# Kernel optimization log

Hardware: AMD Instinct MI355X
Metric: run time of the kernel (lower is better)

## Reference

```python
import jax, jax.numpy as jnp
import numpy as np

DIM = 256; INNER = 512; HEADS = 8; DHEAD = 64; WS = 7; K = 3; EPS = 1e-5

def _rel_idx(ws):
    idx = np.array([[x, y] for x in range(ws) for y in range(ws)])
    d = idx[None, :, :] - idx[:, None, :]
    d[:, :, 0] += ws - 1
    d[:, :, 1] += ws - 1
    d[:, :, 0] *= 2 * ws - 1
    return jnp.asarray(d.sum(-1))  # [ws^2, ws^2] int

REL_IDX = _rel_idx(WS)

def _proj(x, dw, g, b, m, v, pw):
    # depthwise conv (k=3, pad=1, groups=C) -> BN (eval mode) -> 1x1 pointwise
    p = K // 2
    y = jax.lax.conv_general_dilated(x, dw, (1, 1), ((p, p), (p, p)),
                                     feature_group_count=x.shape[1])
    y = (y - m[None, :, None, None]) * jax.lax.rsqrt(v[None, :, None, None] + EPS) \
        * g[None, :, None, None] + b[None, :, None, None]
    return jax.lax.conv_general_dilated(y, pw, (1, 1), 'VALID')

def _windows(t):
    # [b, h*d, H, W] -> [b, h, nw, ws*ws, d]  (non-shuffle partition)
    b, c, H, W = t.shape
    nh, nw = H // WS, W // WS
    t = t.reshape(b, HEADS, DHEAD, nh, WS, nw, WS)
    t = t.transpose(0, 1, 3, 5, 4, 6, 2)  # b h nh nw ws ws d
    return t.reshape(b, HEADS, nh * nw, WS * WS, DHEAD)

def _unwindows(t, H, W):
    b = t.shape[0]
    nh, nw = H // WS, W // WS
    t = t.reshape(b, HEADS, nh, nw, WS, WS, DHEAD)
    t = t.transpose(0, 1, 6, 2, 4, 3, 5)  # b h d nh ws nw ws
    return t.reshape(b, HEADS * DHEAD, H, W)

def setup_inputs() -> dict:
    key = jax.random.key(0)
    ks = jax.random.split(key, 32)
    d = {'x': jax.random.normal(ks[0], (16, DIM, 56, 56), jnp.float32)}
    i = 1
    for p in ('q', 'k', 'v'):
        d[p + '_dw'] = jax.random.normal(ks[i], (DIM, 1, K, K), jnp.float32) * 0.1; i += 1
        d[p + '_g'] = jax.random.uniform(ks[i], (DIM,), jnp.float32); i += 1
        d[p + '_b'] = jax.random.normal(ks[i], (DIM,), jnp.float32) * 0.1; i += 1
        d[p + '_m'] = jax.random.normal(ks[i], (DIM,), jnp.float32) * 0.1; i += 1
        d[p + '_v'] = jax.random.uniform(ks[i], (DIM,), jnp.float32); i += 1
        d[p + '_pw'] = jax.random.normal(ks[i], (INNER, DIM, 1, 1), jnp.float32) * 0.05; i += 1
    d['pos_emb'] = jax.random.normal(ks[i], ((2 * WS - 1) ** 2, HEADS), jnp.float32); i += 1
    d['out_w'] = jax.random.normal(ks[i], (DIM, INNER, 1, 1), jnp.float32) * 0.05; i += 1
    d['out_b'] = jax.random.normal(ks[i], (DIM,), jnp.float32) * 0.1
    return d

def reference(x, q_dw, q_g, q_b, q_m, q_v, q_pw,
              k_dw, k_g, k_b, k_m, k_v, k_pw,
              v_dw, v_g, v_b, v_m, v_v, v_pw,
              pos_emb, out_w, out_b):
    H, W = x.shape[2], x.shape[3]
    q = _windows(_proj(x, q_dw, q_g, q_b, q_m, q_v, q_pw))
    k = _windows(_proj(x, k_dw, k_g, k_b, k_m, k_v, k_pw))
    v = _windows(_proj(x, v_dw, v_g, v_b, v_m, v_v, v_pw))
    dots = jnp.einsum('bhwid,bhwjd->bhwij', q, k) * (DHEAD ** -0.5)
    bias = pos_emb[REL_IDX]              # [i, j, heads]
    dots = dots + bias.transpose(2, 0, 1)[None, :, None]  # broadcast over b, w
    attn = jax.nn.softmax(dots, axis=-1)
    out = jnp.einsum('bhwij,bhwjd->bhwid', attn, v)
    out = _unwindows(out, H, W)
    out = jax.lax.conv_general_dilated(out, out_w, (1, 1), 'VALID') \
          + out_b[None, :, None, None]
    return out
```

## Files before the change

### kernel.cpp

```cpp
#include <hip/hip_runtime.h>
#include <hip/hip_bf16.h>

typedef __hip_bfloat16 bf16;
typedef __bf16 bfv8 __attribute__((ext_vector_type(8)));
typedef float f32x4 __attribute__((ext_vector_type(4)));

constexpr int B_     = 16;
constexpr int C_     = 256;
constexpr int INNER_ = 512;
constexpr int HEADS_ = 8;
constexpr int DH_    = 64;
constexpr int HW_    = 56;
constexpr int NPIX_  = HW_ * HW_;
constexpr int WS_    = 7;
constexpr int WSQ_   = 49;
constexpr int NWIN_  = 64;

static __device__ __forceinline__ void async16(const void* g, void* l) {
    __builtin_amdgcn_global_load_lds(
        (const __attribute__((address_space(1))) unsigned int*)g,
        (__attribute__((address_space(3))) unsigned int*)l, 16, 0, 0);
}

__global__ __launch_bounds__(256) void setup_kernel(
    const float* __restrict__ pw0, const float* __restrict__ pw1,
    const float* __restrict__ pw2, const float* __restrict__ pw3,
    bf16* __restrict__ wq,
    const float* __restrict__ dw0, const float* __restrict__ g0,
    const float* __restrict__ b0, const float* __restrict__ m0,
    const float* __restrict__ v0,
    const float* __restrict__ dw1, const float* __restrict__ g1,
    const float* __restrict__ b1, const float* __restrict__ m1,
    const float* __restrict__ v1,
    const float* __restrict__ dw2, const float* __restrict__ g2,
    const float* __restrict__ b2, const float* __restrict__ m2,
    const float* __restrict__ v2,
    float* __restrict__ wf,
    const float* __restrict__ pos, float* __restrict__ biasf) {
    int bx = blockIdx.x;
    if (bx < 2048) {
        int g = bx >> 9;
        const float* s = g == 0 ? pw0 : (g == 1 ? pw1 : (g == 2 ? pw2 : pw3));
        int i = (bx & 511) * 256 + threadIdx.x;
        wq[(size_t)g * (INNER_ * C_) + i] = __float2bfloat16(s[i]);
    } else if (bx < 2051) {
        int p = bx - 2048, c = threadIdx.x;
        const float* dw = p == 0 ? dw0 : (p == 1 ? dw1 : dw2);
        const float* g  = p == 0 ? g0  : (p == 1 ? g1  : g2);
        const float* bb = p == 0 ? b0  : (p == 1 ? b1  : b2);
        const float* mm = p == 0 ? m0  : (p == 1 ? m1  : m2);
        const float* vv = p == 0 ? v0  : (p == 1 ? v1  : v2);
        float s = g[c] * rsqrtf(vv[c] + 1e-5f);
        float* o = wf + (size_t)(p * 256 + c) * 12;
#pragma unroll
        for (int k = 0; k < 9; ++k) o[k] = dw[c * 9 + k] * s;
        o[9] = bb[c] - mm[c] * s;
        o[10] = 0.f; o[11] = 0.f;
    } else {
        int h = bx - 2051;
        int wv = threadIdx.x >> 6, lane = threadIdx.x & 63;
        int quad = lane >> 4, col16 = lane & 15;
        float* dst = biasf + (((size_t)h * 4 + wv) * 64 + lane) * 16;
#pragma unroll
        for (int nt = 0; nt < 4; ++nt)
#pragma unroll
            for (int r = 0; r < 4; ++r) {
                int row = wv * 16 + quad * 4 + r;
                int col = nt * 16 + col16;
                float v;
                if (col >= WSQ_) v = -1e30f;
                else if (row >= WSQ_) v = 0.f;
                else {
                    int xi = row / WS_, yi = row % WS_;
                    int xj = col / WS_, yj = col % WS_;
                    int rel = (xj - xi + 6) * 13 + (yj - yi + 6);
                    v = pos[rel * HEADS_ + h];
                }
                dst[nt * 4 + r] = v;
            }
    }
}

__global__ __launch_bounds__(256) void dwbn3_kernel(
    const float* __restrict__ x, const float* __restrict__ wf,
    bf16* __restrict__ tq, bf16* __restrict__ tk, bf16* __restrict__ tv) {
    __shared__ float xs[3 * 64 * 61];
    int y  = blockIdx.x;
    int c0 = blockIdx.y * 64;
    int b  = blockIdx.z;
    int tid = threadIdx.x;
    for (int i = tid; i < 2688; i += 256) {
        int row = i / 896;
        int rem = i - row * 896;
        int ch = rem / 14, s = rem - ch * 14;
        int yy = y + row - 1;
        float4 v4 = make_float4(0.f, 0.f, 0.f, 0.f);
        if (yy >= 0 && yy < HW_)
            v4 = *(const float4*)(x + (size_t)(b * C_ + c0 + ch) * NPIX_
                                    + yy * HW_ + s * 4);
        float* d = xs + (row * 64 + ch) * 61 + 1 + s * 4;
        d[0] = v4.x; d[1] = v4.y; d[2] = v4.z; d[3] = v4.w;
    }
    for (int j = tid; j < 192; j += 256) {
        int row = j >> 6, ch = j & 63;
        xs[(row * 64 + ch) * 61] = 0.f;
        xs[(row * 64 + ch) * 61 + 57] = 0.f;
    }
    __syncthreads();

    int cg = tid & 31, xo = tid >> 5;
    int bcol = xo * 7;
    unsigned int pack[3][7];
#pragma unroll
    for (int ci = 0; ci < 2; ++ci) {
        int ch = cg * 2 + ci;
        float4 w[3][3];
#pragma unroll
        for (int p = 0; p < 3; ++p) {
            const float* wp = wf + (size_t)(p * 256 + c0 + ch) * 12;
            w[p][0] = *(const float4*)(wp);
            w[p][1] = *(const float4*)(wp + 4);
            w[p][2] = *(const float4*)(wp + 8);
        }
        const float* r0 = xs + ch * 61;
        const float* r1 = r0 + 64 * 61;
        const float* r2 = r1 + 64 * 61;
        float a00 = r0[bcol], a01 = r0[bcol + 1];
        float a10 = r1[bcol], a11 = r1[bcol + 1];
        float a20 = r2[bcol], a21 = r2[bcol + 1];
#pragma unroll
        for (int px = 0; px < 7; ++px) {
            float a02 = r0[bcol + px + 2];
            float a12 = r1[bcol + px + 2];
            float a22 = r2[bcol + px + 2];
#pragma unroll
            for (int p = 0; p < 3; ++p) {
                float acc = w[p][2].y
                    + w[p][0].x * a00 + w[p][0].y * a01 + w[p][0].z * a02
                    + w[p][0].w * a10 + w[p][1].x * a11 + w[p][1].y * a12
                    + w[p][1].z * a20 + w[p][1].w * a21 + w[p][2].x * a22;
                bf16 hv = __float2bfloat16(acc);
                unsigned short u; __builtin_memcpy(&u, &hv, 2);
                if (ci == 0) pack[p][px] = u;
                else         pack[p][px] |= ((unsigned int)u) << 16;
            }
            a00 = a01; a01 = a02; a10 = a11; a11 = a12; a20 = a21; a21 = a22;
        }
    }
    bf16* outs[3] = {tq, tk, tv};
    size_t pbase = ((size_t)b * NPIX_ + y * HW_ + bcol) * C_ + c0 + cg * 2;
#pragma unroll
    for (int p = 0; p < 3; ++p)
#pragma unroll
        for (int px = 0; px < 7; ++px)
            *(unsigned int*)(outs[p] + pbase + px * C_) = pack[p][px];
}

__global__ __launch_bounds__(256) void gemm_qkv_mfma(
    const bf16* __restrict__ Wbase, const bf16* __restrict__ Tbase,
    bf16* __restrict__ Qbase) {
    __shared__ __align__(16) char smem[128 * 136 * 2];
    bf16* sA = (bf16*)smem;
    bf16* sB = sA + 128 * 32;
    bf16* sC = (bf16*)smem;
    int tid = threadIdx.x;
    int c0 = blockIdx.x * 128;
    int p0 = blockIdx.y * 128;
    int zp = blockIdx.z >> 4;
    int b  = blockIdx.z & 15;
    const bf16* W = Wbase + (size_t)zp * (INNER_ * C_);
    const bf16* T = Tbase + (size_t)zp * ((size_t)B_ * NPIX_ * C_);
    bf16* Q = Qbase + (size_t)zp * ((size_t)B_ * INNER_ * NPIX_);
    float qscale = (zp == 0) ? 0.125f : 1.0f;

    int row0 = tid >> 2;
    int kc   = (tid & 3) * 8;
    int pA0 = p0 + row0;       if (pA0 > NPIX_ - 1) pA0 = NPIX_ - 1;
    int pA1 = p0 + row0 + 64;  if (pA1 > NPIX_ - 1) pA1 = NPIX_ - 1;
    const bf16* gA0 = T + ((size_t)b * NPIX_ + pA0) * 256 + kc;
    const bf16* gA1 = T + ((size_t)b * NPIX_ + pA1) * 256 + kc;
    const bf16* gB0 = W + (size_t)(c0 + row0) * 256 + kc;
    const bf16* gB1 = W + (size_t)(c0 + row0 + 64) * 256 + kc;
    char* lA = (char*)sA + tid * 16;
    char* lB = (char*)sB + tid * 16;

    int lane = tid & 63, wv = tid >> 6;
    int wm = (wv >> 1) * 64;
    int wn = (wv & 1) * 64;
    int col16 = lane & 15, quad = lane >> 4;

    f32x4 acc[4][4] = {};
    for (int k0 = 0; k0 < 256; k0 += 32) {
        async16(gA0, lA);
        async16(gA1, lA + 4096);
        async16(gB0, lB);
        async16(gB1, lB + 4096);
        gA0 += 32; gA1 += 32; gB0 += 32; gB1 += 32;
        __syncthreads();
        bfv8 af[4], bfr[4];
#pragma unroll
        for (int mt = 0; mt < 4; ++mt)
            af[mt] = *(const bfv8*)(sA + (wm + mt * 16 + col16) * 32 + quad * 8);
#pragma unroll
        for (int nt = 0; nt < 4; ++nt)
            bfr[nt] = *(const bfv8*)(sB + (wn + nt * 16 + col16) * 32 + quad * 8);
#pragma unroll
        for (int mt = 0; mt < 4; ++mt)
#pragma unroll
            for (int nt = 0; nt < 4; ++nt)
                acc[mt][nt] = __builtin_amdgcn_mfma_f32_16x16x32_bf16(
                    af[mt], bfr[nt], acc[mt][nt], 0, 0, 0);
        __syncthreads();
    }
#pragma unroll
    for (int mt = 0; mt < 4; ++mt)
#pragma unroll
        for (int nt = 0; nt < 4; ++nt) {
            f32x4 a = acc[mt][nt];
#pragma unroll
            for (int r = 0; r < 4; ++r)
                sC[(wm + mt * 16 + quad * 4 + r) * 136 + wn + nt * 16 + col16] =
                    __float2bfloat16(a[r] * qscale);
        }
    __syncthreads();
#pragma unroll
    for (int j = 0; j < 8; ++j) {
        int lin = j * 256 + tid;
        int pixl = lin >> 4, chg = lin & 15;
        int p = p0 + pixl;
        if (p < NPIX_) {
            int ch = c0 + chg * 8;
            int h = ch >> 6, d = ch & 63;
            int yy = p / HW_, xx = p % HW_;
            int wdw = (yy / WS_) * 8 + (xx / WS_);
            int j49 = (yy % WS_) * WS_ + (xx % WS_);
            bfv8 vd = *(const bfv8*)(sC + pixl * 136 + chg * 8);
            *(bfv8*)(Q + ((((size_t)b * HEADS_ + h) * NWIN_ + wdw) * WSQ_ + j49) * DH_ + d) = vd;
        }
    }
}

__global__ __launch_bounds__(256) void attn_mfma(
    const bf16* __restrict__ Q, const bf16* __restrict__ Kt,
    const bf16* __restrict__ V, const float* __restrict__ biasf,
    bf16* __restrict__ O) {
    __shared__ __align__(16) bf16 qs[64 * 72];
    __shared__ __align__(16) bf16 ks[64 * 72];
    __shared__ __align__(16) bf16 vt[64 * 72];
    bf16* ps = qs;
    int tid = threadIdx.x;
    int w = blockIdx.x & 63;
    int h = (blockIdx.x >> 6) & 7;
    int b = blockIdx.x >> 9;
    size_t base = (((size_t)b * HEADS_ + h) * NWIN_ + w) * (WSQ_ * DH_);

    {
        bfv8 z = {};
#pragma unroll
        for (int it = 0; it < 2; ++it) {
            int c = it * 256 + tid;
            int row = c >> 3, col = (c & 7) * 8;
            bfv8 vq = z, vk = z;
            if (c < 392) {
                vq = *(const bfv8*)(Q + base + c * 8);
                vk = *(const bfv8*)(Kt + base + c * 8);
            }
            *(bfv8*)(qs + row * 72 + col) = vq;
            *(bfv8*)(ks + row * 72 + col) = vk;
        }
#pragma unroll
        for (int it = 0; it < 2; ++it) {
            int idx = it * 256 + tid;
            int d = idx & 63, j8 = idx >> 6;
            bf16 val[8];
            if (j8 < 6) {
#pragma unroll
                for (int u = 0; u < 8; ++u)
                    val[u] = V[base + (j8 * 8 + u) * 64 + d];
            } else {
#pragma unroll
                for (int u = 0; u < 8; ++u) {
                    int j = j8 * 8 + u;
                    val[u] = (j < WSQ_) ? V[base + j * 64 + d]
                                        : __float2bfloat16(0.f);
                }
            }
            *(bfv8*)(vt + d * 72 + j8 * 8) = *(const bfv8*)val;
        }
    }
    __syncthreads();

    int lane = tid & 63, wv = tid >> 6;
    int band = wv * 16;
    int col16 = lane & 15, quad = lane >> 4;

    bfv8 aq0 = *(const bfv8*)(qs + (band + col16) * 72 + quad * 8);
    bfv8 aq1 = *(const bfv8*)(qs + (band + col16) * 72 + 32 + quad * 8);
    bfv8 bk[4][2];
#pragma unroll
    for (int nt = 0; nt < 4; ++nt) {
        bk[nt][0] = *(const bfv8*)(ks + (nt * 16 + col16) * 72 + quad * 8);
        bk[nt][1] = *(const bfv8*)(ks + (nt * 16 + col16) * 72 + 32 + quad * 8);
    }
    __syncthreads();

    const float* bp = biasf + (((size_t)h * 4 + wv) * 64 + lane) * 16;
    f32x4 sacc[4];
#pragma unroll
    for (int nt = 0; nt < 4; ++nt) {
        sacc[nt] = *(const f32x4*)(bp + nt * 4);
        sacc[nt] = __builtin_amdgcn_mfma_f32_16x16x32_bf16(aq0, bk[nt][0], sacc[nt], 0, 0, 0);
        sacc[nt] = __builtin_amdgcn_mfma_f32_16x16x32_bf16(aq1, bk[nt][1], sacc[nt], 0, 0, 0);
    }
    float p[4][4];
    float inv[4];
#pragma unroll
    for (int r = 0; r < 4; ++r) {
        float s0 = sacc[0][r], s1 = sacc[1][r], s2 = sacc[2][r], s3 = sacc[3][r];
        float mx = fmaxf(fmaxf(s0, s1), fmaxf(s2, s3));
        mx = fmaxf(mx, __shfl_xor(mx, 1, 16));
        mx = fmaxf(mx, __shfl_xor(mx, 2, 16));
        mx = fmaxf(mx, __shfl_xor(mx, 4, 16));
        mx = fmaxf(mx, __shfl_xor(mx, 8, 16));
        float e0 = __expf(s0 - mx), e1 = __expf(s1 - mx);
        float e2 = __expf(s2 - mx), e3 = __expf(s3 - mx);
        float sm = e0 + e1 + e2 + e3;
        sm += __shfl_xor(sm, 1, 16);
        sm += __shfl_xor(sm, 2, 16);
        sm += __shfl_xor(sm, 4, 16);
        sm += __shfl_xor(sm, 8, 16);
        p[0][r] = e0; p[1][r] = e1; p[2][r] = e2; p[3][r] = e3;
        inv[r] = 1.f / sm;
    }
#pragma unroll
    for (int nt = 0; nt < 4; ++nt)
#pragma unroll
        for (int r = 0; r < 4; ++r)
            ps[(band + quad * 4 + r) * 72 + nt * 16 + col16] = __float2bfloat16(p[nt][r]);
    f32x4 oacc[4] = {};
    bfv8 ap0 = *(const bfv8*)(ps + (band + col16) * 72 + quad * 8);
    bfv8 ap1 = *(const bfv8*)(ps + (band + col16) * 72 + 32 + quad * 8);
#pragma unroll
    for (int nt = 0; nt < 4; ++nt) {
        bfv8 bv0 = *(const bfv8*)(vt + (nt * 16 + col16) * 72 + quad * 8);
        bfv8 bv1 = *(const bfv8*)(vt + (nt * 16 + col16) * 72 + 32 + quad * 8);
        oacc[nt] = __builtin_amdgcn_mfma_f32_16x16x32_bf16(ap0, bv0, oacc[nt], 0, 0, 0);
        oacc[nt] = __builtin_amdgcn_mfma_f32_16x16x32_bf16(ap1, bv1, oacc[nt], 0, 0, 0);
    }
    int wy = w >> 3, wx = w & 7;
#pragma unroll
    for (int r = 0; r < 4; ++r) {
        int i = band + quad * 4 + r;
        if (i < WSQ_) {
            int py = wy * WS_ + i / WS_, px = wx * WS_ + i % WS_;
            size_t ob = ((size_t)b * NPIX_ + py * HW_ + px) * INNER_ + h * DH_;
            float sc = inv[r];
#pragma unroll
            for (int nt = 0; nt < 4; ++nt)
                O[ob + nt * 16 + col16] = __float2bfloat16(oacc[nt][r] * sc);
        }
    }
}

__global__ __launch_bounds__(256) void gemm_out_mfma(
    const bf16* __restrict__ W, const bf16* __restrict__ O,
    const float* __restrict__ bias, float* __restrict__ out) {
    __shared__ __align__(16) bf16 sA[128 * 32];
    __shared__ __align__(16) bf16 sB[128 * 32];
    int tid = threadIdx.x;
    int c0 = blockIdx.x * 128;
    int p0 = blockIdx.y * 128;
    int b  = blockIdx.z;

    int row0 = tid >> 2;
    int kc   = (tid & 3) * 8;
    int pB0 = p0 + row0;       if (pB0 > NPIX_ - 1) pB0 = NPIX_ - 1;
    int pB1 = p0 + row0 + 64;  if (pB1 > NPIX_ - 1) pB1 = NPIX_ - 1;
    const bf16* gA0 = W + (size_t)(c0 + row0) * 512 + kc;
    const bf16* gA1 = W + (size_t)(c0 + row0 + 64) * 512 + kc;
    const bf16* gB0 = O + ((size_t)b * NPIX_ + pB0) * 512 + kc;
    const bf16* gB1 = O + ((size_t)b * NPIX_ + pB1) * 512 + kc;
    char* lA = (char*)sA + tid * 16;
    char* lB = (char*)sB + tid * 16;

    int lane = tid & 63, wv = tid >> 6;
    int wm = (wv >> 1) * 64;
    int wn = (wv & 1) * 64;
    int col16 = lane & 15, quad = lane >> 4;

    f32x4 acc[4][4] = {};
    for (int k0 = 0; k0 < 512; k0 += 32) {
        async16(gA0, lA);
        async16(gA1, lA + 4096);
        async16(gB0, lB);
        async16(gB1, lB + 4096);
        gA0 += 32; gA1 += 32; gB0 += 32; gB1 += 32;
        __syncthreads();
        bfv8 af[4], bfr[4];
#pragma unroll
        for (int mt = 0; mt < 4; ++mt)
            af[mt] = *(const bfv8*)(sA + (wm + mt * 16 + col16) * 32 + quad * 8);
#pragma unroll
        for (int nt = 0; nt < 4; ++nt)
            bfr[nt] = *(const bfv8*)(sB + (wn + nt * 16 + col16) * 32 + quad * 8);
#pragma unroll
        for (int mt = 0; mt < 4; ++mt)
#pragma unroll
            for (int nt = 0; nt < 4; ++nt)
                acc[mt][nt] = __builtin_amdgcn_mfma_f32_16x16x32_bf16(
                    af[mt], bfr[nt], acc[mt][nt], 0, 0, 0);
        __syncthreads();
    }
#pragma unroll
    for (int mt = 0; mt < 4; ++mt) {
#pragma unroll
        for (int r = 0; r < 4; ++r) {
            int ch = c0 + wm + mt * 16 + quad * 4 + r;
            float bc = bias[ch];
#pragma unroll
            for (int nt = 0; nt < 4; ++nt) {
                int p = p0 + wn + nt * 16 + col16;
                if (p < NPIX_)
                    out[((size_t)b * C_ + ch) * NPIX_ + p] = acc[mt][nt][r] + bc;
            }
        }
    }
}

extern "C" void kernel_launch(void* const* d_in, const int* in_sizes, int n_in,
                              void* d_out, int out_size, void* d_ws, size_t ws_size,
                              hipStream_t stream) {
    (void)in_sizes; (void)n_in; (void)out_size; (void)ws_size;
    const float* x     = (const float*)d_in[0];
    const float* pos   = (const float*)d_in[19];
    const float* out_w = (const float*)d_in[20];
    const float* out_b = (const float*)d_in[21];

    size_t tElems = (size_t)B_ * NPIX_ * C_;
    size_t qElems = (size_t)B_ * INNER_ * NPIX_;
    bf16* tq = (bf16*)d_ws;
    bf16* q  = tq + 3 * tElems;
    bf16* o  = tq;
    float* wf = (float*)(q + 3 * qElems);
    bf16* wq = (bf16*)(wf + 3 * 256 * 12);
    bf16* wo = wq + 3 * (INNER_ * C_);
    float* biasf = (float*)(wo + C_ * INNER_);

    dim3 blk(256);
    dim3 gDw(HW_, 4, B_);
    dim3 gQkv(INNER_ / 128, 25, 3 * B_);
    dim3 gOut(C_ / 128, 25, B_);

    setup_kernel<<<2059, blk, 0, stream>>>(
        (const float*)d_in[6], (const float*)d_in[12], (const float*)d_in[18],
        out_w, wq,
        (const float*)d_in[1],  (const float*)d_in[2],  (const float*)d_in[3],
        (const float*)d_in[4],  (const float*)d_in[5],
        (const float*)d_in[7],  (const float*)d_in[8],  (const float*)d_in[9],
        (const float*)d_in[10], (const float*)d_in[11],
        (const float*)d_in[13], (const float*)d_in[14], (const float*)d_in[15],
        (const float*)d_in[16], (const float*)d_in[17], wf,
        pos, biasf);

    dwbn3_kernel<<<gDw, blk, 0, stream>>>(x, wf, tq, tq + tElems, tq + 2 * tElems);
    gemm_qkv_mfma<<<gQkv, blk, 0, stream>>>(wq, tq, q);
    attn_mfma<<<B_ * HEADS_ * NWIN_, blk, 0, stream>>>(
        q, q + qElems, q + 2 * qElems, biasf, o);
    gemm_out_mfma<<<gOut, blk, 0, stream>>>(wo, o, out_b, (float*)d_out);
}
```

Baseline: 358.2 us.

## Enlarge QKV GEMM tile to 256 pixels and remap blocks for L2 locality

The QKV projection GEMM tile grows from 128x128 to 256 pixels x 128 channels, so each wave computes 128x64 outputs with 8x4 MFMA accumulators. This gives more reuse of the loaded weight tile per pixel. The block index is linearised and swizzled so that groups of 8 consecutive blocks share channel tiles, aiming at better L2 reuse. The epilogue writes the two 128-row halves through shared memory one after the other. In exchange, register pressure doubles, which may reduce occupancy, and there are fewer blocks (2496 vs 4800), which gives a worse tail on the last pixel tile.

```diff
diff --git a/kernel.cpp b/kernel.cpp
--- a/kernel.cpp
+++ b/kernel.cpp
@@ -161,13 +161,21 @@
     bf16* __restrict__ Qbase) {
     __shared__ __align__(16) char smem[128 * 136 * 2];
     bf16* sA = (bf16*)smem;
-    bf16* sB = sA + 128 * 32;
+    bf16* sB = sA + 256 * 32;
     bf16* sC = (bf16*)smem;
     int tid = threadIdx.x;
-    int c0 = blockIdx.x * 128;
-    int p0 = blockIdx.y * 128;
-    int zp = blockIdx.z >> 4;
-    int b  = blockIdx.z & 15;
+    int lin = blockIdx.x + (blockIdx.y << 2) + blockIdx.z * 52;
+    int s  = lin & 7;
+    int u  = lin >> 3;
+    int ch_t = u & 3;
+    int v  = u >> 2;
+    int pz = v * 8 + s;
+    int pix_t = pz % 13;
+    int z     = pz / 13;
+    int zp = z >> 4;
+    int b  = z & 15;
+    int c0 = ch_t * 128;
+    int p0 = pix_t * 256;
     const bf16* W = Wbase + (size_t)zp * (INNER_ * C_);
     const bf16* T = Tbase + (size_t)zp * ((size_t)B_ * NPIX_ * C_);
     bf16* Q = Qbase + (size_t)zp * ((size_t)B_ * INNER_ * NPIX_);
@@ -175,37 +183,43 @@
 
     int row0 = tid >> 2;
     int kc   = (tid & 3) * 8;
-    int pA0 = p0 + row0;       if (pA0 > NPIX_ - 1) pA0 = NPIX_ - 1;
-    int pA1 = p0 + row0 + 64;  if (pA1 > NPIX_ - 1) pA1 = NPIX_ - 1;
-    const bf16* gA0 = T + ((size_t)b * NPIX_ + pA0) * 256 + kc;
-    const bf16* gA1 = T + ((size_t)b * NPIX_ + pA1) * 256 + kc;
+    const bf16* gA[4];
+#pragma unroll
+    for (int it = 0; it < 4; ++it) {
+        int pA = p0 + row0 + it * 64;
+        if (pA > NPIX_ - 1) pA = NPIX_ - 1;
+        gA[it] = T + ((size_t)b * NPIX_ + pA) * 256 + kc;
+    }
     const bf16* gB0 = W + (size_t)(c0 + row0) * 256 + kc;
     const bf16* gB1 = W + (size_t)(c0 + row0 + 64) * 256 + kc;
     char* lA = (char*)sA + tid * 16;
     char* lB = (char*)sB + tid * 16;
 
     int lane = tid & 63, wv = tid >> 6;
-    int wm = (wv >> 1) * 64;
+    int wm = (wv >> 1) * 128;
     int wn = (wv & 1) * 64;
     int col16 = lane & 15, quad = lane >> 4;
 
-    f32x4 acc[4][4] = {};
+    f32x4 acc[8][4] = {};
     for (int k0 = 0; k0 < 256; k0 += 32) {
-        async16(gA0, lA);
-        async16(gA1, lA + 4096);
+#pragma unroll
+        for (int it = 0; it < 4; ++it) {
+            async16(gA[it], lA + it * 4096);
+            gA[it] += 32;
+        }
         async16(gB0, lB);
         async16(gB1, lB + 4096);
-        gA0 += 32; gA1 += 32; gB0 += 32; gB1 += 32;
-        __syncthreads();
-        bfv8 af[4], bfr[4];
-#pragma unroll
-        for (int mt = 0; mt < 4; ++mt)
+        gB0 += 32; gB1 += 32;
+        __syncthreads();
+        bfv8 af[8], bfr[4];
+#pragma unroll
+        for (int mt = 0; mt < 8; ++mt)
             af[mt] = *(const bfv8*)(sA + (wm + mt * 16 + col16) * 32 + quad * 8);
 #pragma unroll
         for (int nt = 0; nt < 4; ++nt)
             bfr[nt] = *(const bfv8*)(sB + (wn + nt * 16 + col16) * 32 + quad * 8);
 #pragma unroll
-        for (int mt = 0; mt < 4; ++mt)
+        for (int mt = 0; mt < 8; ++mt)
 #pragma unroll
             for (int nt = 0; nt < 4; ++nt)
                 acc[mt][nt] = __builtin_amdgcn_mfma_f32_16x16x32_bf16(
@@ -213,30 +227,36 @@
         __syncthreads();
     }
 #pragma unroll
-    for (int mt = 0; mt < 4; ++mt)
-#pragma unroll
-        for (int nt = 0; nt < 4; ++nt) {
-            f32x4 a = acc[mt][nt];
-#pragma unroll
-            for (int r = 0; r < 4; ++r)
-                sC[(wm + mt * 16 + quad * 4 + r) * 136 + wn + nt * 16 + col16] =
-                    __float2bfloat16(a[r] * qscale);
-        }
-    __syncthreads();
-#pragma unroll
-    for (int j = 0; j < 8; ++j) {
-        int lin = j * 256 + tid;
-        int pixl = lin >> 4, chg = lin & 15;
-        int p = p0 + pixl;
-        if (p < NPIX_) {
-            int ch = c0 + chg * 8;
-            int h = ch >> 6, d = ch & 63;
-            int yy = p / HW_, xx = p % HW_;
-            int wdw = (yy / WS_) * 8 + (xx / WS_);
-            int j49 = (yy % WS_) * WS_ + (xx % WS_);
-            bfv8 vd = *(const bfv8*)(sC + pixl * 136 + chg * 8);
-            *(bfv8*)(Q + ((((size_t)b * HEADS_ + h) * NWIN_ + wdw) * WSQ_ + j49) * DH_ + d) = vd;
-        }
+    for (int h2 = 0; h2 < 2; ++h2) {
+        if ((wv >> 1) == h2) {
+#pragma unroll
+            for (int mt = 0; mt < 8; ++mt)
+#pragma unroll
+                for (int nt = 0; nt < 4; ++nt) {
+                    f32x4 a = acc[mt][nt];
+#pragma unroll
+                    for (int r = 0; r < 4; ++r)
+                        sC[(mt * 16 + quad * 4 + r) * 136 + wn + nt * 16 + col16] =
+                            __float2bfloat16(a[r] * qscale);
+                }
+        }
+        __syncthreads();
+#pragma unroll
+        for (int j = 0; j < 8; ++j) {
+            int lin2 = j * 256 + tid;
+            int pixl = lin2 >> 4, chg = lin2 & 15;
+            int p = p0 + h2 * 128 + pixl;
+            if (p < NPIX_) {
+                int ch = c0 + chg * 8;
+                int h = ch >> 6, d = ch & 63;
+                int yy = p / HW_, xx = p % HW_;
+                int wdw = (yy / WS_) * 8 + (xx / WS_);
+                int j49 = (yy % WS_) * WS_ + (xx % WS_);
+                bfv8 vd = *(const bfv8*)(sC + pixl * 136 + chg * 8);
+                *(bfv8*)(Q + ((((size_t)b * HEADS_ + h) * NWIN_ + wdw) * WSQ_ + j49) * DH_ + d) = vd;
+            }
+        }
+        __syncthreads();
     }
 }
 
@@ -448,7 +468,7 @@
 
     dim3 blk(256);
     dim3 gDw(HW_, 4, B_);
-    dim3 gQkv(INNER_ / 128, 25, 3 * B_);
+    dim3 gQkv(4, 13, 48);
     dim3 gOut(C_ / 128, 25, B_);
 
     setup_kernel<<<2059, blk, 0, stream>>>(
```

Result: slower. 402.8 us (+12.5%).
